# Kernel tuning notes

Measured on AMD Instinct MI355X. Metric: run time of the kernel, lower is better.

## Reference

```python
import jax, jax.numpy as jnp
import numpy as np

N_HEADS = 16
HEAD_DIM = 128  # d_model // n_heads


def rope(x):
    # x: [B, H, T, D]. Matches the torch module: interleaved even/odd split,
    # then concat([x1*cos - x2*sin, x1*sin + x2*cos], axis=-1).
    T, D = x.shape[2], x.shape[3]
    inv_freq = 1.0 / (10000.0 ** (jnp.arange(0, D, 2, dtype=x.dtype) / D))  # [D/2]
    freqs = jnp.arange(T, dtype=x.dtype)[:, None] * inv_freq[None, :]       # [T, D/2]
    sin, cos = jnp.sin(freqs), jnp.cos(freqs)                               # [T, D/2]
    x1, x2 = x[..., ::2], x[..., 1::2]                                      # [B,H,T,D/2]
    return jnp.concatenate([x1 * cos - x2 * sin, x1 * sin + x2 * cos], axis=-1)


def setup_inputs() -> dict:
    key = jax.random.key(0)
    ks = jax.random.split(key, 5)
    B, T, C = 2, 2048, 2048
    scale = 1.0 / np.sqrt(C)
    return {
        "x": jax.random.normal(ks[0], (B, T, C), dtype=jnp.float32),
        "W_qkv": jax.random.normal(ks[1], (3 * C, C), dtype=jnp.float32) * scale,
        "b_qkv": jnp.zeros((3 * C,), dtype=jnp.float32),
        "W_out": jax.random.normal(ks[2], (C, C), dtype=jnp.float32) * scale,
        "b_out": jnp.zeros((C,), dtype=jnp.float32),
    }


def reference(x, W_qkv, b_qkv, W_out, b_out):
    B, T, C = x.shape
    H, D = N_HEADS, HEAD_DIM
    qkv = x @ W_qkv.T + b_qkv                      # [B, T, 3C]
    qkv = qkv.reshape(B, T, 3, H, D)
    q, k, v = qkv[:, :, 0], qkv[:, :, 1], qkv[:, :, 2]  # [B, T, H, D]
    q = rope(jnp.transpose(q, (0, 2, 1, 3)))       # [B, H, T, D]
    k = rope(jnp.transpose(k, (0, 2, 1, 3)))
    v = jnp.transpose(v, (0, 2, 1, 3))
    scores = jnp.einsum("bhqd,bhkd->bhqk", q, k) / jnp.sqrt(jnp.asarray(D, x.dtype))
    causal = jnp.tril(jnp.ones((T, T), dtype=bool))
    scores = jnp.where(causal, scores, jnp.finfo(x.dtype).min)
    attn = jax.nn.softmax(scores, axis=-1)
    out = jnp.einsum("bhqk,bhkd->bhqd", attn, v)   # [B, H, T, D]
    out = jnp.transpose(out, (0, 2, 1, 3)).reshape(B, T, C)
    return out @ W_out.T + b_out
```

## Files before the change

### kernel.cpp

```cpp
#include <hip/hip_runtime.h>
#include <hip/hip_bf16.h>

typedef __attribute__((ext_vector_type(8))) short bf16x8;
typedef __attribute__((ext_vector_type(4))) float f32x4;

#define GLOAD_LDS16(gptr, lptr) \
  __builtin_amdgcn_global_load_lds((const __attribute__((address_space(1))) void*)(gptr), \
                                   (__attribute__((address_space(3))) void*)(lptr), 16, 0, 0)

__device__ __forceinline__ unsigned short f2b(float f) {
  union { float f; unsigned u; } x; x.f = f;
  unsigned r = x.u + 0x7fffu + ((x.u >> 16) & 1u);
  return (unsigned short)(r >> 16);
}
__device__ __forceinline__ float b2f(unsigned short u) {
  union { unsigned u; float f; } x; x.u = ((unsigned)u) << 16;
  return x.f;
}

__global__ void cast_kernel(const float* __restrict__ in, unsigned short* __restrict__ out, int n) {
  const int i = (blockIdx.x * 256 + threadIdx.x) * 4;
  if (i < n) {
    const float4 v = *(const float4*)(in + i);
    ushort4 r;
    r.x = f2b(v.x); r.y = f2b(v.y); r.z = f2b(v.z); r.w = f2b(v.w);
    *(ushort4*)(out + i) = r;
  }
}

template<int OUTF32>
__global__ __launch_bounds__(512, 2)
void gemm256(const unsigned short* __restrict__ A,
             const unsigned short* __restrict__ Bm,
             const float* __restrict__ bias,
             void* __restrict__ Cp,
             int M, int N, int K)
{
  __shared__ __align__(16) char Lds[131072];
  const int t  = threadIdx.x;
  const int l  = t & 63;
  const int w  = t >> 6;
  const int lr = l & 15;
  const int lkb = (l >> 4) << 4;
  const int wr = w >> 2;
  const int wc = w & 3;

  const int nwg = gridDim.x;
  const int wg  = (blockIdx.x & 7) * (nwg >> 3) + (blockIdx.x >> 3);
  const int NBN = N >> 8;
  const int bm = wg / NBN, bn = wg % NBN;

  const int sw3 = (lr & 7) << 4;
  const int ck0 = lkb ^ sw3;
  const int ck1 = (64 | lkb) ^ sw3;

  const int lb0 = t << 4;
  const int lb1 = lb0 + 8192;
  const int d0 = lb0 ^ (((lb0 >> 7) & 7) << 4);
  const int d1 = lb1 ^ (((lb1 >> 7) & 7) << 4);
  const long K2 = (long)K * 2;
  const char* Ab = (const char*)A  + (long)(bm * 256) * K2;
  const char* Bb = (const char*)Bm + (long)(bn * 256) * K2;
  const long s0 = (long)(d0 >> 7) * K2 + (d0 & 127);
  const long s1 = (long)(d1 >> 7) * K2 + (d1 & 127);
  const long hstep = (long)128 * K2;

  auto stageA = [&](int g, int h) {
    char* dst = Lds + (g & 1) * 65536 + h * 16384;
    const char* src = Ab + (long)h * hstep + (long)g * 128;
    GLOAD_LDS16(src + s0, dst + lb0);
    GLOAD_LDS16(src + s1, dst + lb1);
  };
  auto stageB = [&](int g, int h) {
    char* dst = Lds + (g & 1) * 65536 + 32768 + h * 16384;
    const char* src = Bb + (long)h * hstep + (long)g * 128;
    GLOAD_LDS16(src + s0, dst + lb0);
    GLOAD_LDS16(src + s1, dst + lb1);
  };

  f32x4 acc[8][4] = {};
  const int NT = K >> 6;
  const int brow = ((wc & 1) * 64 + lr) << 7;

  bf16x8 af[4][2], blo[2][2], bhi[2][2];

  stageA(0, 0); stageA(0, 1);
  stageB(0, 0); stageB(0, 1);
  stageB(1, 0); stageB(1, 1);
  asm volatile("s_waitcnt vmcnt(4)" ::: "memory");
  __builtin_amdgcn_s_barrier();
  {
    const char* AH0 = Lds + wr * 16384;
    const char* BH0 = Lds + 32768 + (wc >> 1) * 16384;
#pragma unroll
    for (int ni = 0; ni < 2; ++ni) {
      blo[ni][0] = *(const bf16x8*)(BH0 + brow + (ni << 11) + ck0);
      blo[ni][1] = *(const bf16x8*)(BH0 + brow + (ni << 11) + ck1);
    }
#pragma unroll
    for (int mi = 0; mi < 4; ++mi) {
      af[mi][0] = *(const bf16x8*)(AH0 + ((mi * 16 + lr) << 7) + ck0);
      af[mi][1] = *(const bf16x8*)(AH0 + ((mi * 16 + lr) << 7) + ck1);
    }
#pragma unroll
    for (int ni = 0; ni < 2; ++ni) {
      bhi[ni][0] = *(const bf16x8*)(BH0 + brow + ((ni + 2) << 11) + ck0);
      bhi[ni][1] = *(const bf16x8*)(BH0 + brow + ((ni + 2) << 11) + ck1);
    }
  }

  for (int tt = 0; tt < NT; ++tt) {
    const char* SB = Lds + (tt & 1) * 65536;
    const char* AH = SB + wr * 16384;

    if (tt + 1 < NT) { stageA(tt + 1, 0); stageA(tt + 1, 1); }
    __builtin_amdgcn_s_barrier();
    __builtin_amdgcn_sched_barrier(0);
    __builtin_amdgcn_s_setprio(1);
#pragma unroll
    for (int mi = 0; mi < 4; ++mi)
#pragma unroll
      for (int ni = 0; ni < 2; ++ni) {
        acc[mi][ni] = __builtin_amdgcn_mfma_f32_16x16x32_bf16(af[mi][0], blo[ni][0], acc[mi][ni], 0, 0, 0);
        acc[mi][ni] = __builtin_amdgcn_mfma_f32_16x16x32_bf16(af[mi][1], blo[ni][1], acc[mi][ni], 0, 0, 0);
      }
    __builtin_amdgcn_s_setprio(0);
    __builtin_amdgcn_s_barrier();
    __builtin_amdgcn_sched_barrier(0);

    __builtin_amdgcn_s_setprio(1);
#pragma unroll
    for (int mi = 0; mi < 4; ++mi)
#pragma unroll
      for (int ni = 0; ni < 2; ++ni) {
        acc[mi][ni + 2] = __builtin_amdgcn_mfma_f32_16x16x32_bf16(af[mi][0], bhi[ni][0], acc[mi][ni + 2], 0, 0, 0);
        acc[mi][ni + 2] = __builtin_amdgcn_mfma_f32_16x16x32_bf16(af[mi][1], bhi[ni][1], acc[mi][ni + 2], 0, 0, 0);
      }
    __builtin_amdgcn_s_setprio(0);
#pragma unroll
    for (int mi = 0; mi < 4; ++mi) {
      af[mi][0] = *(const bf16x8*)(AH + ((64 + mi * 16 + lr) << 7) + ck0);
      af[mi][1] = *(const bf16x8*)(AH + ((64 + mi * 16 + lr) << 7) + ck1);
    }
    __builtin_amdgcn_s_barrier();
    __builtin_amdgcn_sched_barrier(0);

    asm volatile("s_waitcnt vmcnt(0)" ::: "memory");
    if (tt + 2 < NT) stageB(tt + 2, 0);
    __builtin_amdgcn_s_setprio(1);
#pragma unroll
    for (int mi = 0; mi < 4; ++mi)
#pragma unroll
      for (int ni = 0; ni < 2; ++ni) {
        acc[mi + 4][ni] = __builtin_amdgcn_mfma_f32_16x16x32_bf16(af[mi][0], blo[ni][0], acc[mi + 4][ni], 0, 0, 0);
        acc[mi + 4][ni] = __builtin_amdgcn_mfma_f32_16x16x32_bf16(af[mi][1], blo[ni][1], acc[mi + 4][ni], 0, 0, 0);
      }
    __builtin_amdgcn_s_setprio(0);
    if (tt + 1 < NT) {
      const char* BHn = Lds + ((tt + 1) & 1) * 65536 + 32768 + (wc >> 1) * 16384;
#pragma unroll
      for (int ni = 0; ni < 2; ++ni) {
        blo[ni][0] = *(const bf16x8*)(BHn + brow + (ni << 11) + ck0);
        blo[ni][1] = *(const bf16x8*)(BHn + brow + (ni << 11) + ck1);
      }
    }
    __builtin_amdgcn_s_barrier();
    __builtin_amdgcn_sched_barrier(0);

    if (tt + 2 < NT) stageB(tt + 2, 1);
    __builtin_amdgcn_s_setprio(1);
#pragma unroll
    for (int mi = 0; mi < 4; ++mi)
#pragma unroll
      for (int ni = 0; ni < 2; ++ni) {
        acc[mi + 4][ni + 2] = __builtin_amdgcn_mfma_f32_16x16x32_bf16(af[mi][0], bhi[ni][0], acc[mi + 4][ni + 2], 0, 0, 0);
        acc[mi + 4][ni + 2] = __builtin_amdgcn_mfma_f32_16x16x32_bf16(af[mi][1], bhi[ni][1], acc[mi + 4][ni + 2], 0, 0, 0);
      }
    __builtin_amdgcn_s_setprio(0);
    if (tt + 1 < NT) {
      const char* SBn = Lds + ((tt + 1) & 1) * 65536;
      const char* AHn = SBn + wr * 16384;
      const char* BHn = SBn + 32768 + (wc >> 1) * 16384;
#pragma unroll
      for (int mi = 0; mi < 4; ++mi) {
        af[mi][0] = *(const bf16x8*)(AHn + ((mi * 16 + lr) << 7) + ck0);
        af[mi][1] = *(const bf16x8*)(AHn + ((mi * 16 + lr) << 7) + ck1);
      }
#pragma unroll
      for (int ni = 0; ni < 2; ++ni) {
        bhi[ni][0] = *(const bf16x8*)(BHn + brow + ((ni + 2) << 11) + ck0);
        bhi[ni][1] = *(const bf16x8*)(BHn + brow + ((ni + 2) << 11) + ck1);
      }
    }
    __builtin_amdgcn_s_barrier();
    __builtin_amdgcn_sched_barrier(0);
  }

  const int roff = (l >> 4) << 2;
  const int row0 = bm * 256 + wr * 128 + roff;
  const int col0 = bn * 256 + wc * 64 + lr;
#pragma unroll
  for (int ni = 0; ni < 4; ++ni) {
    const int col = col0 + ni * 16;
    const float bv = bias ? bias[col] : 0.0f;
#pragma unroll
    for (int mi = 0; mi < 8; ++mi) {
#pragma unroll
      for (int r = 0; r < 4; ++r) {
        const int row = row0 + mi * 16 + r;
        const float v = acc[mi][ni][r] + bv;
        if (OUTF32) ((float*)Cp)[(long)row * N + col] = v;
        else ((unsigned short*)Cp)[(long)row * N + col] = f2b(v);
      }
    }
  }
}

__global__ void rope_kernel(const unsigned short* __restrict__ qkv,
                            unsigned short* __restrict__ Qr,
                            unsigned short* __restrict__ Kr)
{
  const int T = 2048;
  const int idx = blockIdx.x * 256 + threadIdx.x;
  const int d  = idx & 63;
  const int tt = (idx >> 6) & (T - 1);
  const int bh = idx >> 17;
  const int b = bh >> 4, h = bh & 15;
  const long base = ((long)(b * T + tt) * 3) * 2048 + h * 128;
  const float inv = exp2f(-(float)d * 0.2076205059304602f);
  const float fr = (float)tt * inv;
  float sn, cs;
  sincosf(fr, &sn, &cs);
  const float q1 = b2f(qkv[base + 2 * d]);
  const float q2 = b2f(qkv[base + 2 * d + 1]);
  const float k1 = b2f(qkv[base + 2048 + 2 * d]);
  const float k2 = b2f(qkv[base + 2048 + 2 * d + 1]);
  const long ob = ((long)bh * T + tt) * 128;
  Qr[ob + d]      = f2b(q1 * cs - q2 * sn);
  Qr[ob + 64 + d] = f2b(q1 * sn + q2 * cs);
  Kr[ob + d]      = f2b(k1 * cs - k2 * sn);
  Kr[ob + 64 + d] = f2b(k1 * sn + k2 * cs);
}

__global__ void vtrans_kernel(const unsigned short* __restrict__ qkv,
                              unsigned short* __restrict__ Vt)
{
  const int T = 2048;
  __shared__ unsigned short ld[128][65];
  const int bh = blockIdx.y, tt = blockIdx.x;
  const int b = bh >> 4, h = bh & 15;
  const int t = threadIdx.x;
#pragma unroll
  for (int i = 0; i < 32; ++i) {
    const int idx = i * 256 + t;
    const int d = idx & 127, tr = idx >> 7;
    ld[d][tr] = qkv[((long)(b * T + tt * 64 + tr) * 3 + 2) * 2048 + h * 128 + d];
  }
  __syncthreads();
#pragma unroll
  for (int i = 0; i < 32; ++i) {
    const int idx = i * 256 + t;
    const int tc = idx & 63, dr = idx >> 6;
    Vt[((long)bh * 128 + dr) * T + tt * 64 + tc] = ld[dr][tc];
  }
}

__global__ __launch_bounds__(256)
void attn_fwd(const unsigned short* __restrict__ Q,
              const unsigned short* __restrict__ Kg,
              const unsigned short* __restrict__ Vt,
              unsigned short* __restrict__ O, int T)
{
  __shared__ __align__(16) unsigned short Ks[2][64 * 128];
  __shared__ __align__(16) unsigned short Vs[2][128 * 64];
  __shared__ __align__(16) unsigned short Ps[4][16 * 64];
  const int t = threadIdx.x;
  const int w = t >> 6, l = t & 63;
  const int lr = l & 15;
  const int g16 = (l >> 4) << 4;
  const int sw = (lr & 7) << 4;
  const int bh = blockIdx.x;
  const int qt = (gridDim.y - 1) - blockIdx.y;
  const int q0 = qt * 64 + w * 16;
  const long hbase = (long)bh * T * 128;
  const long hbase2 = hbase * 2;
  const long T2 = (long)T * 2;
  const int roff = (l >> 4) << 2;

  bf16x8 qf[4];
  const unsigned short* Qrow = Q + hbase + (long)(q0 + lr) * 128;
#pragma unroll
  for (int ds = 0; ds < 4; ++ds) qf[ds] = *(const bf16x8*)&Qrow[ds * 32 + (g16 >> 1)];

  f32x4 o[8] = {};
  float m[4]    = {-INFINITY, -INFINITY, -INFINITY, -INFINITY};
  float lsum[4] = {0.f, 0.f, 0.f, 0.f};

  auto stage = [&](int kt, int buf) {
#pragma unroll
    for (int c = 0; c < 4; ++c) {
      const int o2 = t * 16 + c * 4096;
      const int krow = o2 >> 8, kcb = o2 & 255;
      GLOAD_LDS16((const char*)Kg + hbase2 + (long)kt * 16384 + krow * 256 + (kcb ^ ((krow & 7) << 4)),
                  (char*)Ks[buf] + o2);
      const int vrow = o2 >> 7, vcb = o2 & 127;
      GLOAD_LDS16((const char*)Vt + (long)(bh * 128 + vrow) * T2 + (long)kt * 128 + (vcb ^ ((vrow & 7) << 4)),
                  (char*)Vs[buf] + o2);
    }
  };

  const int ntile = qt + 1;
  stage(0, 0);
  __syncthreads();

  for (int kt = 0; kt < ntile; ++kt) {
    const int cur = kt & 1;
    if (kt + 1 < ntile) stage(kt + 1, cur ^ 1);

    const char* KsB = (const char*)Ks[cur];
    const char* VsB = (const char*)Vs[cur];

    f32x4 s[4] = {};
    __builtin_amdgcn_s_setprio(1);
#pragma unroll
    for (int tj = 0; tj < 4; ++tj)
#pragma unroll
      for (int ds = 0; ds < 4; ++ds) {
        bf16x8 kf = *(const bf16x8*)(KsB + (tj * 16 + lr) * 256 + ((ds * 64 + g16) ^ sw));
        s[tj] = __builtin_amdgcn_mfma_f32_16x16x32_bf16(qf[ds], kf, s[tj], 0, 0, 0);
      }
    __builtin_amdgcn_s_setprio(0);

    const float scale = 0.08838834764831845f;
#pragma unroll
    for (int tj = 0; tj < 4; ++tj) s[tj] *= scale;
    if (kt == qt) {
#pragma unroll
      for (int tj = 0; tj < 4; ++tj)
#pragma unroll
        for (int j = 0; j < 4; ++j)
          if (kt * 64 + tj * 16 + lr > q0 + roff + j) s[tj][j] = -INFINITY;
    }

    float corr[4];
#pragma unroll
    for (int j = 0; j < 4; ++j) {
      float v = fmaxf(fmaxf(s[0][j], s[1][j]), fmaxf(s[2][j], s[3][j]));
      v = fmaxf(v, __shfl_xor(v, 1, 64));
      v = fmaxf(v, __shfl_xor(v, 2, 64));
      v = fmaxf(v, __shfl_xor(v, 4, 64));
      v = fmaxf(v, __shfl_xor(v, 8, 64));
      const float mn = fmaxf(m[j], v);
      corr[j] = __expf(m[j] - mn);
      m[j] = mn;
    }
    float rs[4] = {0.f, 0.f, 0.f, 0.f};
#pragma unroll
    for (int tj = 0; tj < 4; ++tj)
#pragma unroll
      for (int j = 0; j < 4; ++j) {
        const float p = __expf(s[tj][j] - m[j]);
        rs[j] += p;
        const int prow = roff + j;
        *(unsigned short*)((char*)Ps[w] + prow * 128 + (((tj * 16 + lr) * 2) ^ ((prow & 7) << 4))) = f2b(p);
      }
#pragma unroll
    for (int j = 0; j < 4; ++j) {
      float v = rs[j];
      v += __shfl_xor(v, 1, 64);
      v += __shfl_xor(v, 2, 64);
      v += __shfl_xor(v, 4, 64);
      v += __shfl_xor(v, 8, 64);
      lsum[j] = lsum[j] * corr[j] + v;
    }
#pragma unroll
    for (int nj = 0; nj < 8; ++nj)
#pragma unroll
      for (int j = 0; j < 4; ++j) o[nj][j] *= corr[j];

    __builtin_amdgcn_s_setprio(1);
#pragma unroll
    for (int ks = 0; ks < 2; ++ks) {
      bf16x8 pf = *(const bf16x8*)((const char*)Ps[w] + lr * 128 + ((ks * 64 + g16) ^ sw));
#pragma unroll
      for (int nj = 0; nj < 8; ++nj) {
        bf16x8 vf = *(const bf16x8*)(VsB + (nj * 16 + lr) * 128 + ((ks * 64 + g16) ^ sw));
        o[nj] = __builtin_amdgcn_mfma_f32_16x16x32_bf16(pf, vf, o[nj], 0, 0, 0);
      }
    }
    __builtin_amdgcn_s_setprio(0);
    __syncthreads();
  }

  float inv[4];
#pragma unroll
  for (int j = 0; j < 4; ++j) inv[j] = 1.0f / lsum[j];
  const int b = bh >> 4, h = bh & 15;
#pragma unroll
  for (int nj = 0; nj < 8; ++nj)
#pragma unroll
    for (int j = 0; j < 4; ++j) {
      const int q = q0 + roff + j;
      const int d = nj * 16 + lr;
      O[(long)(b * T + q) * 2048 + h * 128 + d] = f2b(o[nj][j] * inv[j]);
    }
}

extern "C" void kernel_launch(void* const* d_in, const int* in_sizes, int n_in,
                              void* d_out, int out_size, void* d_ws, size_t ws_size,
                              hipStream_t stream)
{
  const int B = 2, T = 2048, C = 2048;
  const int M = B * T;
  const int N1 = 3 * C;
  const float* x    = (const float*)d_in[0];
  const float* Wqkv = (const float*)d_in[1];
  const float* bqkv = (const float*)d_in[2];
  const float* Wout = (const float*)d_in[3];
  const float* bout = (const float*)d_in[4];
  float* out = (float*)d_out;

  char* p = (char*)d_ws;
  unsigned short* xb    = (unsigned short*)p; p += (size_t)M * C * 2;
  unsigned short* wqkvb = (unsigned short*)p; p += (size_t)N1 * C * 2;
  unsigned short* woutb = (unsigned short*)p; p += (size_t)C * C * 2;
  unsigned short* qkv   = (unsigned short*)p; p += (size_t)M * N1 * 2;
  unsigned short* Qr    = (unsigned short*)p; p += (size_t)M * C * 2;
  unsigned short* Kr    = (unsigned short*)p; p += (size_t)M * C * 2;
  unsigned short* Vt    = (unsigned short*)p; p += (size_t)M * C * 2;
  unsigned short* Ob    = xb;

  cast_kernel<<<M * C / 1024, 256, 0, stream>>>(x, xb, M * C);
  cast_kernel<<<N1 * C / 1024, 256, 0, stream>>>(Wqkv, wqkvb, N1 * C);
  cast_kernel<<<C * C / 1024, 256, 0, stream>>>(Wout, woutb, C * C);

  gemm256<0><<<dim3((M / 256) * (N1 / 256)), 512, 0, stream>>>(xb, wqkvb, bqkv, qkv, M, N1, C);

  rope_kernel<<<(32 * T * 64) / 256, 256, 0, stream>>>(qkv, Qr, Kr);
  vtrans_kernel<<<dim3(T / 64, 32), 256, 0, stream>>>(qkv, Vt);

  attn_fwd<<<dim3(32, T / 64), 256, 0, stream>>>(Qr, Kr, Vt, Ob, T);

  gemm256<1><<<dim3((M / 256) * (C / 256)), 512, 0, stream>>>(Ob, woutb, bout, out, M, C, C);
}
```

Measured before the change: 321.0 us.

## Process two query strips per attention block to reuse staged K/V tiles

Each attention block now handles 128 query rows: each wave owns two 16-row strips, 64 rows apart, sharing the same staged K/V tiles in LDS. This halves the number of K/V tile loads per query row and halves the grid size. The softmax also folds the scale and log2(e) into a single constant and uses exp2f instead of __expf. The cost is doubled accumulator registers per wave, which may lower occupancy, and fewer blocks to fill the GPU.

```diff
diff --git a/kernel.cpp b/kernel.cpp
--- a/kernel.cpp
+++ b/kernel.cpp
@@ -281,20 +281,29 @@
   const int sw = (lr & 7) << 4;
   const int bh = blockIdx.x;
   const int qt = (gridDim.y - 1) - blockIdx.y;
-  const int q0 = qt * 64 + w * 16;
+  const int q0a = qt * 128 + w * 16;
+  const int q0b = q0a + 64;
   const long hbase = (long)bh * T * 128;
   const long hbase2 = hbase * 2;
   const long T2 = (long)T * 2;
   const int roff = (l >> 4) << 2;
-
-  bf16x8 qf[4];
-  const unsigned short* Qrow = Q + hbase + (long)(q0 + lr) * 128;
-#pragma unroll
-  for (int ds = 0; ds < 4; ++ds) qf[ds] = *(const bf16x8*)&Qrow[ds * 32 + (g16 >> 1)];
-
-  f32x4 o[8] = {};
-  float m[4]    = {-INFINITY, -INFINITY, -INFINITY, -INFINITY};
-  float lsum[4] = {0.f, 0.f, 0.f, 0.f};
+  const float C1 = 0.08838834764831845f * 1.4426950408889634f;
+
+  bf16x8 qfA[4], qfB[4];
+  {
+    const unsigned short* QrowA = Q + hbase + (long)(q0a + lr) * 128;
+    const unsigned short* QrowB = Q + hbase + (long)(q0b + lr) * 128;
+#pragma unroll
+    for (int ds = 0; ds < 4; ++ds) {
+      qfA[ds] = *(const bf16x8*)&QrowA[ds * 32 + (g16 >> 1)];
+      qfB[ds] = *(const bf16x8*)&QrowB[ds * 32 + (g16 >> 1)];
+    }
+  }
+
+  f32x4 oA[8] = {}, oB[8] = {};
+  float mA[4] = {-INFINITY, -INFINITY, -INFINITY, -INFINITY};
+  float mB[4] = {-INFINITY, -INFINITY, -INFINITY, -INFINITY};
+  float lA[4] = {0.f, 0.f, 0.f, 0.f}, lB[4] = {0.f, 0.f, 0.f, 0.f};
 
   auto stage = [&](int kt, int buf) {
 #pragma unroll
@@ -309,7 +318,7 @@
     }
   };
 
-  const int ntile = qt + 1;
+  const int ntile = 2 * qt + 2;
   stage(0, 0);
   __syncthreads();
 
@@ -320,89 +329,95 @@
     const char* KsB = (const char*)Ks[cur];
     const char* VsB = (const char*)Vs[cur];
 
-    f32x4 s[4] = {};
-    __builtin_amdgcn_s_setprio(1);
-#pragma unroll
-    for (int tj = 0; tj < 4; ++tj)
-#pragma unroll
-      for (int ds = 0; ds < 4; ++ds) {
-        bf16x8 kf = *(const bf16x8*)(KsB + (tj * 16 + lr) * 256 + ((ds * 64 + g16) ^ sw));
-        s[tj] = __builtin_amdgcn_mfma_f32_16x16x32_bf16(qf[ds], kf, s[tj], 0, 0, 0);
-      }
-    __builtin_amdgcn_s_setprio(0);
-
-    const float scale = 0.08838834764831845f;
-#pragma unroll
-    for (int tj = 0; tj < 4; ++tj) s[tj] *= scale;
-    if (kt == qt) {
+    auto strip = [&](const bf16x8* qf, f32x4* o, float* m, float* lsum, int q0s) {
+      f32x4 s[4] = {};
+      __builtin_amdgcn_s_setprio(1);
 #pragma unroll
       for (int tj = 0; tj < 4; ++tj)
 #pragma unroll
-        for (int j = 0; j < 4; ++j)
-          if (kt * 64 + tj * 16 + lr > q0 + roff + j) s[tj][j] = -INFINITY;
-    }
-
-    float corr[4];
+        for (int ds = 0; ds < 4; ++ds) {
+          bf16x8 kf = *(const bf16x8*)(KsB + (tj * 16 + lr) * 256 + ((ds * 64 + g16) ^ sw));
+          s[tj] = __builtin_amdgcn_mfma_f32_16x16x32_bf16(qf[ds], kf, s[tj], 0, 0, 0);
+        }
+      __builtin_amdgcn_s_setprio(0);
+
+      const bool diag = (kt == ((q0s + 15) >> 6));
+      if (diag) {
+#pragma unroll
+        for (int tj = 0; tj < 4; ++tj)
+#pragma unroll
+          for (int j = 0; j < 4; ++j)
+            if (kt * 64 + tj * 16 + lr > q0s + roff + j) s[tj][j] = -INFINITY;
+      }
+
+      float corr[4];
+#pragma unroll
+      for (int j = 0; j < 4; ++j) {
+        float v = fmaxf(fmaxf(s[0][j], s[1][j]), fmaxf(s[2][j], s[3][j]));
+        v = fmaxf(v, __shfl_xor(v, 1, 64));
+        v = fmaxf(v, __shfl_xor(v, 2, 64));
+        v = fmaxf(v, __shfl_xor(v, 4, 64));
+        v = fmaxf(v, __shfl_xor(v, 8, 64));
+        const float mn = fmaxf(m[j], v * C1);
+        corr[j] = exp2f(m[j] - mn);
+        m[j] = mn;
+      }
+      float rs[4] = {0.f, 0.f, 0.f, 0.f};
+#pragma unroll
+      for (int tj = 0; tj < 4; ++tj)
+#pragma unroll
+        for (int j = 0; j < 4; ++j) {
+          const float p = exp2f(fmaf(s[tj][j], C1, -m[j]));
+          rs[j] += p;
+          const int prow = roff + j;
+          *(unsigned short*)((char*)Ps[w] + prow * 128 + (((tj * 16 + lr) * 2) ^ ((prow & 7) << 4))) = f2b(p);
+        }
+#pragma unroll
+      for (int j = 0; j < 4; ++j) {
+        float v = rs[j];
+        v += __shfl_xor(v, 1, 64);
+        v += __shfl_xor(v, 2, 64);
+        v += __shfl_xor(v, 4, 64);
+        v += __shfl_xor(v, 8, 64);
+        lsum[j] = lsum[j] * corr[j] + v;
+      }
+#pragma unroll
+      for (int nj = 0; nj < 8; ++nj)
+#pragma unroll
+        for (int j = 0; j < 4; ++j) o[nj][j] *= corr[j];
+
+      __builtin_amdgcn_s_setprio(1);
+#pragma unroll
+      for (int ks = 0; ks < 2; ++ks) {
+        bf16x8 pf = *(const bf16x8*)((const char*)Ps[w] + lr * 128 + ((ks * 64 + g16) ^ sw));
+#pragma unroll
+        for (int nj = 0; nj < 8; ++nj) {
+          bf16x8 vf = *(const bf16x8*)(VsB + (nj * 16 + lr) * 128 + ((ks * 64 + g16) ^ sw));
+          o[nj] = __builtin_amdgcn_mfma_f32_16x16x32_bf16(pf, vf, o[nj], 0, 0, 0);
+        }
+      }
+      __builtin_amdgcn_s_setprio(0);
+    };
+
+    if (kt <= 2 * qt) strip(qfA, oA, mA, lA, q0a);
+    strip(qfB, oB, mB, lB, q0b);
+
+    __syncthreads();
+  }
+
+  const int b = bh >> 4, h = bh & 15;
+  float invA[4], invB[4];
+#pragma unroll
+  for (int j = 0; j < 4; ++j) { invA[j] = 1.0f / lA[j]; invB[j] = 1.0f / lB[j]; }
+#pragma unroll
+  for (int nj = 0; nj < 8; ++nj)
 #pragma unroll
     for (int j = 0; j < 4; ++j) {
-      float v = fmaxf(fmaxf(s[0][j], s[1][j]), fmaxf(s[2][j], s[3][j]));
-      v = fmaxf(v, __shfl_xor(v, 1, 64));
-      v = fmaxf(v, __shfl_xor(v, 2, 64));
-      v = fmaxf(v, __shfl_xor(v, 4, 64));
-      v = fmaxf(v, __shfl_xor(v, 8, 64));
-      const float mn = fmaxf(m[j], v);
-      corr[j] = __expf(m[j] - mn);
-      m[j] = mn;
-    }
-    float rs[4] = {0.f, 0.f, 0.f, 0.f};
-#pragma unroll
-    for (int tj = 0; tj < 4; ++tj)
-#pragma unroll
-      for (int j = 0; j < 4; ++j) {
-        const float p = __expf(s[tj][j] - m[j]);
-        rs[j] += p;
-        const int prow = roff + j;
-        *(unsigned short*)((char*)Ps[w] + prow * 128 + (((tj * 16 + lr) * 2) ^ ((prow & 7) << 4))) = f2b(p);
-      }
-#pragma unroll
-    for (int j = 0; j < 4; ++j) {
-      float v = rs[j];
-      v += __shfl_xor(v, 1, 64);
-      v += __shfl_xor(v, 2, 64);
-      v += __shfl_xor(v, 4, 64);
-      v += __shfl_xor(v, 8, 64);
-      lsum[j] = lsum[j] * corr[j] + v;
-    }
-#pragma unroll
-    for (int nj = 0; nj < 8; ++nj)
-#pragma unroll
-      for (int j = 0; j < 4; ++j) o[nj][j] *= corr[j];
-
-    __builtin_amdgcn_s_setprio(1);
-#pragma unroll
-    for (int ks = 0; ks < 2; ++ks) {
-      bf16x8 pf = *(const bf16x8*)((const char*)Ps[w] + lr * 128 + ((ks * 64 + g16) ^ sw));
-#pragma unroll
-      for (int nj = 0; nj < 8; ++nj) {
-        bf16x8 vf = *(const bf16x8*)(VsB + (nj * 16 + lr) * 128 + ((ks * 64 + g16) ^ sw));
-        o[nj] = __builtin_amdgcn_mfma_f32_16x16x32_bf16(pf, vf, o[nj], 0, 0, 0);
-      }
-    }
-    __builtin_amdgcn_s_setprio(0);
-    __syncthreads();
-  }
-
-  float inv[4];
-#pragma unroll
-  for (int j = 0; j < 4; ++j) inv[j] = 1.0f / lsum[j];
-  const int b = bh >> 4, h = bh & 15;
-#pragma unroll
-  for (int nj = 0; nj < 8; ++nj)
-#pragma unroll
-    for (int j = 0; j < 4; ++j) {
-      const int q = q0 + roff + j;
       const int d = nj * 16 + lr;
-      O[(long)(b * T + q) * 2048 + h * 128 + d] = f2b(o[nj][j] * inv[j]);
+      const int qa = q0a + roff + j;
+      O[(long)(b * T + qa) * 2048 + h * 128 + d] = f2b(oA[nj][j] * invA[j]);
+      const int qb = q0b + roff + j;
+      O[(long)(b * T + qb) * 2048 + h * 128 + d] = f2b(oB[nj][j] * invB[j]);
     }
 }
 
@@ -439,7 +454,7 @@
   rope_kernel<<<(32 * T * 64) / 256, 256, 0, stream>>>(qkv, Qr, Kr);
   vtrans_kernel<<<dim3(T / 64, 32), 256, 0, stream>>>(qkv, Vt);
 
-  attn_fwd<<<dim3(32, T / 64), 256, 0, stream>>>(Qr, Kr, Vt, Ob, T);
+  attn_fwd<<<dim3(32, T / 128), 256, 0, stream>>>(Qr, Kr, Vt, Ob, T);
 
   gemm256<1><<<dim3((M / 256) * (C / 256)), 512, 0, stream>>>(Ob, woutb, bout, out, M, C, C);
 }
```

New measurement: 370.6 us. 15.5% more time.
